# Kernel optimization log

Hardware: AMD Instinct MI355X
Metric: run time of the kernel (lower is better)

Reference implementation:

```python
import math
import jax, jax.numpy as jnp
import numpy as np

BLOCK = 256
LAYER_IDX = 5
NUM_HIDDEN_LAYERS = 32


def get_slopes(head_dim):
    equ = lambda x: 1 / 2 ** (8 / x)
    log2 = math.log2(head_dim)
    if log2.is_integer():
        return [equ(head_dim) ** i for i in range(1, head_dim + 1)]
    lower = 2 ** math.floor(log2)
    upper = 2 ** math.ceil(log2)
    ls = get_slopes(lower)
    us = get_slopes(upper)
    return ls + us[::2][: head_dim - lower]


def setup_inputs() -> dict:
    key = jax.random.key(0)
    k1, k2, k3 = jax.random.split(key, 3)
    B, H, S, D = 2, 64, 4096, 64
    q = jax.random.normal(k1, (B, H, S, D), dtype=jnp.float32)
    k = jax.random.normal(k2, (B, H, S, D), dtype=jnp.float32)
    v = jax.random.normal(k3, (B, H, S, D), dtype=jnp.float32)
    mask = jnp.ones((B, S), dtype=jnp.int32)
    return {"query_states": q, "key_states": k, "value_states": v, "attention_mask": mask}


def _lightning_attention(q, k, v, attention_mask):
    B, H, S, D = q.shape
    E = v.shape[-1]
    # mask padded positions in values
    v = v * attention_mask[:, None, :, None].astype(v.dtype)

    # per-head decay slopes, scaled by layer depth (note: H == D by construction)
    slopes = np.asarray(get_slopes(D), dtype=np.float32)
    slopes = slopes * (1.0 - LAYER_IDX / (NUM_HIDDEN_LAYERS - 1) + 1e-05)
    slope = jnp.asarray(slopes)[:, None, None]  # [H, 1, 1]

    arr = jnp.arange(1, BLOCK + 1, dtype=jnp.float32)
    q_decay = jnp.exp(-slope * arr[:, None])            # [H, BLOCK, 1]
    k_decay = jnp.exp(-slope * (BLOCK - arr)[:, None])  # [H, BLOCK, 1]
    idx = arr[:, None] - arr[None, :]                   # [BLOCK, BLOCK]
    s_idx = slope * idx[None]                           # [H, BLOCK, BLOCK] (slope [H,1,1] broadcasts)
    diag_decay = jnp.exp(jnp.where(idx[None] >= 0, -s_idx, -jnp.inf))  # [H, BLOCK, BLOCK]
    block_decay = jnp.exp(-slope * BLOCK)               # [H, 1, 1]

    nb = S // BLOCK
    qb = q.reshape(B, H, nb, BLOCK, D).transpose(2, 0, 1, 3, 4)  # [nb, B, H, BLOCK, D]
    kb = k.reshape(B, H, nb, BLOCK, D).transpose(2, 0, 1, 3, 4)
    vb = v.reshape(B, H, nb, BLOCK, E).transpose(2, 0, 1, 3, 4)

    def step(kv, blk):
        qi, ki, vi = blk  # each [B, H, BLOCK, D/E]
        # inter-block: decayed query reads recurrent kv state
        o_inter = jnp.einsum('bhmd,bhde->bhme', qi * q_decay, kv)
        # intra-block: causal decayed attention within the block
        qk = jnp.einsum('bhmd,bhnd->bhmn', qi, ki) * diag_decay
        o_intra = jnp.einsum('bhmn,bhne->bhme', qk, vi)
        # update recurrent state
        kv_new = block_decay * kv + jnp.einsum('bhmd,bhme->bhde', ki * k_decay, vi)
        return kv_new, o_inter + o_intra

    kv0 = jnp.zeros((B, H, D, E), dtype=jnp.float32)
    _, outs = jax.lax.scan(step, kv0, (qb, kb, vb))  # outs: [nb, B, H, BLOCK, E]
    out = outs.transpose(1, 2, 0, 3, 4).reshape(B, H, S, E)
    return out


def reference(query_states, key_states, value_states, attention_mask):
    return _lightning_attention(query_states, key_states, value_states, attention_mask)
```

## Files before the change

kernel.cpp:

```cpp
#include <hip/hip_runtime.h>

typedef __attribute__((ext_vector_type(4))) float f4;
typedef __attribute__((ext_vector_type(4))) float f32x4;
typedef __attribute__((ext_vector_type(8))) short short8;
typedef __attribute__((ext_vector_type(4))) short short4v;
typedef __attribute__((ext_vector_type(4))) unsigned int uint4v;

#define S_  4096
#define NB_ 16
#define SLOPE_SCALE 0.838719677419355f

__device__ __forceinline__ float slope_for_head(int h) {
    return exp2f(-(float)(h + 1) * 0.125f) * SLOPE_SCALE;
}

__device__ __forceinline__ short f2bf(float f) {
    unsigned u = __float_as_uint(f);
    u += 0x7FFFu + ((u >> 16) & 1u);
    return (short)(u >> 16);
}

__global__ __launch_bounds__(256, 4) void phase1_kvblocks(
    const float* __restrict__ k, const float* __restrict__ v,
    const int* __restrict__ mask, float* __restrict__ kvt,
    short* __restrict__ vt)
{
    __shared__ float ks[64][68];
    __shared__ float vs[64][68];
    const int j  = blockIdx.x;
    const int bh = blockIdx.y;
    const int b  = bh >> 6;
    const int h  = bh & 63;
    const int t  = threadIdx.x;
    const float slope = slope_for_head(h);
    const int e  = t >> 2;
    const int dg = (t & 3) << 4;

    const f32x4 zf = {0.f, 0.f, 0.f, 0.f};
    f4 acc[4];
    acc[0] = zf; acc[1] = zf; acc[2] = zf; acc[3] = zf;

    const long long tilebase = ((long long)bh * S_ + j * 256) * 64;

    for (int c = 0; c < 4; ++c) {
        for (int i = 0; i < 4; ++i) {
            int fi  = t + i * 256;
            int row = fi >> 4;
            int col = (fi & 15) << 2;
            long long g = tilebase + (long long)(c * 64 + row) * 64 + col;
            *(f4*)&ks[row][col] = *(const f4*)(k + g);
            f4 vv = *(const f4*)(v + g);
            float mv = (float)mask[b * S_ + j * 256 + c * 64 + row];
            vv *= mv;
            *(f4*)&vs[row][col] = vv;
        }
        __syncthreads();

        for (int n = 0; n < 64; ++n) {
            float kd = __expf(-slope * (float)(255 - (c * 64 + n)));
            float a  = vs[n][e] * kd;
            const f4* krow = (const f4*)&ks[n][dg];
            acc[0] += a * krow[0];
            acc[1] += a * krow[1];
            acc[2] += a * krow[2];
            acc[3] += a * krow[3];
        }

        {
            int nb = (t & 3) << 4;
            unsigned w[8];
            for (int i = 0; i < 8; ++i) {
                unsigned lo = (unsigned short)f2bf(vs[nb + 2 * i][e]);
                unsigned hi = (unsigned short)f2bf(vs[nb + 2 * i + 1][e]);
                w[i] = lo | (hi << 16);
            }
            long long g = ((long long)(bh * 64 + e)) * S_ + j * 256 + c * 64 + nb;
            uint4v* dst = (uint4v*)(vt + g);
            uint4v w0 = {w[0], w[1], w[2], w[3]};
            uint4v w1 = {w[4], w[5], w[6], w[7]};
            dst[0] = w0;
            dst[1] = w1;
        }
        __syncthreads();
    }

    float* o = kvt + ((long long)(bh * NB_ + j)) * 4096 + e * 64 + dg;
    *(f4*)(o + 0)  = acc[0];
    *(f4*)(o + 4)  = acc[1];
    *(f4*)(o + 8)  = acc[2];
    *(f4*)(o + 12) = acc[3];
}

__global__ __launch_bounds__(256) void phase2_scan(float* __restrict__ kvt)
{
    const int bh = blockIdx.x;
    const int h  = bh & 63;
    const int t  = threadIdx.x;
    const float slope = slope_for_head(h);
    const float bd = __expf(-slope * 256.0f);

    const f32x4 zf = {0.f, 0.f, 0.f, 0.f};
    f4 st[4];
    st[0] = zf; st[1] = zf; st[2] = zf; st[3] = zf;

    f4* base = (f4*)(kvt + (long long)bh * NB_ * 4096);
    for (int j = 0; j < NB_; ++j) {
        f4* p = base + j * 1024;
        for (int i = 0; i < 4; ++i) {
            f4 tmp = p[t + i * 256];
            p[t + i * 256] = st[i];
            st[i] = st[i] * bd + tmp;
        }
    }
}

__global__ __launch_bounds__(256, 2) void phase3_output(
    const float* __restrict__ q, const float* __restrict__ k,
    const float* __restrict__ kvt, const short* __restrict__ vt,
    float* __restrict__ out)
{
    __shared__ short P[4][64 * 56];
    const int j    = blockIdx.x;
    const int bh   = blockIdx.y;
    const int h    = bh & 63;
    const int tid  = threadIdx.x;
    const int wave = tid >> 6;
    const int lane = tid & 63;
    const int quad = lane >> 4;
    const int l16  = lane & 15;
    const int wrole  = (wave + j) & 3;
    const float slope = slope_for_head(h);
    const int mwbase = wrole << 6;

    const long long rowbase = (long long)bh * S_ + j * 256 + mwbase;

    short8 qf[4][2];
    for (int mt = 0; mt < 4; ++mt) {
        const float* qp = q + (rowbase + mt * 16 + l16) * 64 + quad * 8;
        for (int ks = 0; ks < 2; ++ks) {
            f4 a = *(const f4*)(qp + ks * 32);
            f4 b = *(const f4*)(qp + ks * 32 + 4);
            short8 f;
            f[0] = f2bf(a.x); f[1] = f2bf(a.y); f[2] = f2bf(a.z); f[3] = f2bf(a.w);
            f[4] = f2bf(b.x); f[5] = f2bf(b.y); f[6] = f2bf(b.z); f[7] = f2bf(b.w);
            qf[mt][ks] = f;
        }
    }

    const f32x4 zf = {0.f, 0.f, 0.f, 0.f};
    f32x4 of[4][4];
    for (int et = 0; et < 4; ++et)
        for (int mt = 0; mt < 4; ++mt) of[et][mt] = zf;

    const float* kvp = kvt + ((long long)(bh * NB_ + j) << 12);
    for (int et = 0; et < 4; ++et) {
        for (int ks = 0; ks < 2; ++ks) {
            const float* p = kvp + (et * 16 + l16) * 64 + ks * 32 + quad * 8;
            f4 a = *(const f4*)(p);
            f4 b = *(const f4*)(p + 4);
            short8 af;
            af[0] = f2bf(a.x); af[1] = f2bf(a.y); af[2] = f2bf(a.z); af[3] = f2bf(a.w);
            af[4] = f2bf(b.x); af[5] = f2bf(b.y); af[6] = f2bf(b.z); af[7] = f2bf(b.w);
            for (int mt = 0; mt < 4; ++mt)
                of[et][mt] = __builtin_amdgcn_mfma_f32_16x16x32_bf16(
                    af, qf[mt][ks], of[et][mt], 0, 0, 0);
        }
    }
    for (int mt = 0; mt < 4; ++mt) {
        float qd = __expf(-slope * (float)(mwbase + mt * 16 + l16 + 1));
        for (int et = 0; et < 4; ++et) of[et][mt] *= qd;
    }

    const float er1 = __expf(slope);
    const float er2 = er1 * er1;
    const float er3 = er2 * er1;
    short* Pw = &P[wave][0];
    const int nchunks = (mwbase >> 5) + 2;

    for (int c = 0; c < nchunks; ++c) {
        const int nbase = c << 5;

        short8 kf[2][2];
        for (int nt = 0; nt < 2; ++nt) {
            const float* kp = k + ((long long)bh * S_ + j * 256 + nbase + nt * 16 + l16) * 64 + quad * 8;
            for (int ks = 0; ks < 2; ++ks) {
                f4 a = *(const f4*)(kp + ks * 32);
                f4 b = *(const f4*)(kp + ks * 32 + 4);
                short8 f;
                f[0] = f2bf(a.x); f[1] = f2bf(a.y); f[2] = f2bf(a.z); f[3] = f2bf(a.w);
                f[4] = f2bf(b.x); f[5] = f2bf(b.y); f[6] = f2bf(b.z); f[7] = f2bf(b.w);
                kf[nt][ks] = f;
            }
        }

        f32x4 sf[2][4];
        for (int nt = 0; nt < 2; ++nt)
            for (int mt = 0; mt < 4; ++mt) sf[nt][mt] = zf;
        for (int nt = 0; nt < 2; ++nt)
            for (int ks = 0; ks < 2; ++ks)
                for (int mt = 0; mt < 4; ++mt)
                    sf[nt][mt] = __builtin_amdgcn_mfma_f32_16x16x32_bf16(
                        kf[nt][ks], qf[mt][ks], sf[nt][mt], 0, 0, 0);

        for (int nt = 0; nt < 2; ++nt) {
            for (int mt = 0; mt < 4; ++mt) {
                int n0 = nbase + nt * 16 + quad * 4;
                int m  = mwbase + mt * 16 + l16;
                float ddb = __expf(-slope * (float)(m - n0));
                f32x4 s = sf[nt][mt];
                float v0 = (m >= n0)     ? s[0] * ddb       : 0.f;
                float v1 = (m >= n0 + 1) ? s[1] * ddb * er1 : 0.f;
                float v2 = (m >= n0 + 2) ? s[2] * ddb * er2 : 0.f;
                float v3 = (m >= n0 + 3) ? s[3] * ddb * er3 : 0.f;
                short4v pk = {f2bf(v0), f2bf(v1), f2bf(v2), f2bf(v3)};
                *(short4v*)&Pw[(mt * 16 + l16) * 56 + nt * 16 + quad * 4] = pk;
            }
        }
        asm volatile("s_waitcnt lgkmcnt(0)" ::: "memory");

        short8 pb[4];
        for (int mt = 0; mt < 4; ++mt)
            pb[mt] = *(const short8*)&Pw[(mt * 16 + l16) * 56 + quad * 8];
        short8 va[4];
        for (int et = 0; et < 4; ++et)
            va[et] = *(const short8*)(vt + ((long long)(bh * 64 + et * 16 + l16)) * S_
                                         + j * 256 + nbase + quad * 8);

        for (int et = 0; et < 4; ++et)
            for (int mt = 0; mt < 4; ++mt)
                of[et][mt] = __builtin_amdgcn_mfma_f32_16x16x32_bf16(
                    va[et], pb[mt], of[et][mt], 0, 0, 0);
    }

    for (int mt = 0; mt < 4; ++mt) {
        float* orow = out + (rowbase + mt * 16 + l16) * 64;
        for (int et = 0; et < 4; ++et) {
            f4 o = {of[et][mt][0], of[et][mt][1], of[et][mt][2], of[et][mt][3]};
            *(f4*)(orow + et * 16 + quad * 4) = o;
        }
    }
}

extern "C" void kernel_launch(void* const* d_in, const int* in_sizes, int n_in,
                              void* d_out, int out_size, void* d_ws, size_t ws_size,
                              hipStream_t stream) {
    const float* q    = (const float*)d_in[0];
    const float* k    = (const float*)d_in[1];
    const float* v    = (const float*)d_in[2];
    const int*   mask = (const int*)d_in[3];
    float* kvt = (float*)d_ws;
    short* vt  = (short*)((char*)d_ws + (size_t)128 * 16 * 4096 * 4);
    float* out = (float*)d_out;

    phase1_kvblocks<<<dim3(16, 128), 256, 0, stream>>>(k, v, mask, kvt, vt);
    phase2_scan<<<128, 256, 0, stream>>>(kvt);
    phase3_output<<<dim3(16, 128), 256, 0, stream>>>(q, k, kvt, vt, out);
}
```

Before: 546.5 us.

## Use split-bf16 MFMA for KV blocks, cache bf16 K, split output waves

Phase 1 now computes the per-block K^T V state with MFMA, using a hi/lo bf16 split (three products) to keep near-fp32 accuracy. The k-decay is folded into the shared-memory load, and V^T is stored in a chunk-tiled layout. When the workspace is large enough, phase 1 also writes a bf16 copy of K so phase 3 skips reconverting it. Phase 2 spreads the scan over four times as many blocks and loads all 16 states up front. Phase 3 runs one wave per block with independent row roles, which trades shared-memory reuse for finer scheduling and costs extra writes of the bf16 K copy.

```diff
diff --git a/kernel.cpp b/kernel.cpp
--- a/kernel.cpp
+++ b/kernel.cpp
@@ -19,28 +19,32 @@
     u += 0x7FFFu + ((u >> 16) & 1u);
     return (short)(u >> 16);
 }
-
+__device__ __forceinline__ float bf2f(short s) {
+    return __uint_as_float(((unsigned)(unsigned short)s) << 16);
+}
+
+template<int USE_KBF>
 __global__ __launch_bounds__(256, 4) void phase1_kvblocks(
     const float* __restrict__ k, const float* __restrict__ v,
     const int* __restrict__ mask, float* __restrict__ kvt,
-    short* __restrict__ vt)
+    short* __restrict__ vt, short* __restrict__ kbf)
 {
-    __shared__ float ks[64][68];
-    __shared__ float vs[64][68];
+    __shared__ float ks[64][69];
+    __shared__ float vs[64][69];
     const int j  = blockIdx.x;
     const int bh = blockIdx.y;
     const int b  = bh >> 6;
     const int h  = bh & 63;
     const int t  = threadIdx.x;
+    const int wave = t >> 6, lane = t & 63, quad = lane >> 4, l16 = lane & 15;
     const float slope = slope_for_head(h);
-    const int e  = t >> 2;
-    const int dg = (t & 3) << 4;
 
     const f32x4 zf = {0.f, 0.f, 0.f, 0.f};
-    f4 acc[4];
+    f32x4 acc[4];
     acc[0] = zf; acc[1] = zf; acc[2] = zf; acc[3] = zf;
 
     const long long tilebase = ((long long)bh * S_ + j * 256) * 64;
+    const long long vtbase   = ((long long)(bh * NB_ + j)) * 16384;
 
     for (int c = 0; c < 4; ++c) {
         for (int i = 0; i < 4; ++i) {
@@ -48,95 +52,122 @@
             int row = fi >> 4;
             int col = (fi & 15) << 2;
             long long g = tilebase + (long long)(c * 64 + row) * 64 + col;
-            *(f4*)&ks[row][col] = *(const f4*)(k + g);
+            f4 kk = *(const f4*)(k + g);
+            if (USE_KBF) {
+                short4v kb = { f2bf(kk.x), f2bf(kk.y), f2bf(kk.z), f2bf(kk.w) };
+                *(short4v*)(kbf + g) = kb;
+            }
+            float kd = __expf(-slope * (float)(255 - (c * 64 + row)));
+            *(f4*)&ks[row][col] = kk * kd;
             f4 vv = *(const f4*)(v + g);
             float mv = (float)mask[b * S_ + j * 256 + c * 64 + row];
-            vv *= mv;
-            *(f4*)&vs[row][col] = vv;
+            *(f4*)&vs[row][col] = vv * mv;
         }
         __syncthreads();
 
-        for (int n = 0; n < 64; ++n) {
-            float kd = __expf(-slope * (float)(255 - (c * 64 + n)));
-            float a  = vs[n][e] * kd;
-            const f4* krow = (const f4*)&ks[n][dg];
-            acc[0] += a * krow[0];
-            acc[1] += a * krow[1];
-            acc[2] += a * krow[2];
-            acc[3] += a * krow[3];
-        }
-
         {
+            int e  = t >> 2;
             int nb = (t & 3) << 4;
             unsigned w[8];
-            for (int i = 0; i < 8; ++i) {
-                unsigned lo = (unsigned short)f2bf(vs[nb + 2 * i][e]);
-                unsigned hi = (unsigned short)f2bf(vs[nb + 2 * i + 1][e]);
-                w[i] = lo | (hi << 16);
-            }
-            long long g = ((long long)(bh * 64 + e)) * S_ + j * 256 + c * 64 + nb;
+            #pragma unroll
+            for (int i2 = 0; i2 < 8; ++i2) {
+                unsigned lo = (unsigned short)f2bf(vs[nb + 2 * i2][e]);
+                unsigned hi = (unsigned short)f2bf(vs[nb + 2 * i2 + 1][e]);
+                w[i2] = lo | (hi << 16);
+            }
+            long long g = vtbase + (long long)(c * 2 + (nb >> 5)) * 2048
+                        + e * 32 + (nb & 31);
             uint4v* dst = (uint4v*)(vt + g);
             uint4v w0 = {w[0], w[1], w[2], w[3]};
             uint4v w1 = {w[4], w[5], w[6], w[7]};
-            dst[0] = w0;
-            dst[1] = w1;
+            dst[0] = w0; dst[1] = w1;
+        }
+
+        #pragma unroll
+        for (int cc = 0; cc < 2; ++cc) {
+            const int nb32 = cc * 32;
+            short8 ahi, alo;
+            #pragma unroll
+            for (int jj = 0; jj < 8; ++jj) {
+                float x = vs[nb32 + quad * 8 + jj][wave * 16 + l16];
+                short hi = f2bf(x);
+                ahi[jj] = hi;
+                alo[jj] = f2bf(x - bf2f(hi));
+            }
+            #pragma unroll
+            for (int dt = 0; dt < 4; ++dt) {
+                short8 bhi, blo;
+                #pragma unroll
+                for (int jj = 0; jj < 8; ++jj) {
+                    float x = ks[nb32 + quad * 8 + jj][dt * 16 + l16];
+                    short hi = f2bf(x);
+                    bhi[jj] = hi;
+                    blo[jj] = f2bf(x - bf2f(hi));
+                }
+                acc[dt] = __builtin_amdgcn_mfma_f32_16x16x32_bf16(ahi, bhi, acc[dt], 0, 0, 0);
+                acc[dt] = __builtin_amdgcn_mfma_f32_16x16x32_bf16(ahi, blo, acc[dt], 0, 0, 0);
+                acc[dt] = __builtin_amdgcn_mfma_f32_16x16x32_bf16(alo, bhi, acc[dt], 0, 0, 0);
+            }
         }
         __syncthreads();
     }
 
-    float* o = kvt + ((long long)(bh * NB_ + j)) * 4096 + e * 64 + dg;
-    *(f4*)(o + 0)  = acc[0];
-    *(f4*)(o + 4)  = acc[1];
-    *(f4*)(o + 8)  = acc[2];
-    *(f4*)(o + 12) = acc[3];
+    float* o = kvt + ((long long)(bh * NB_ + j)) * 4096;
+    #pragma unroll
+    for (int dt = 0; dt < 4; ++dt) {
+        #pragma unroll
+        for (int r = 0; r < 4; ++r) {
+            int e = wave * 16 + quad * 4 + r;
+            o[e * 64 + dt * 16 + l16] = acc[dt][r];
+        }
+    }
 }
 
 __global__ __launch_bounds__(256) void phase2_scan(float* __restrict__ kvt)
 {
-    const int bh = blockIdx.x;
-    const int h  = bh & 63;
-    const int t  = threadIdx.x;
+    const int g    = blockIdx.x;
+    const int bh   = g >> 2;
+    const int part = g & 3;
+    const int h    = bh & 63;
     const float slope = slope_for_head(h);
     const float bd = __expf(-slope * 256.0f);
 
-    const f32x4 zf = {0.f, 0.f, 0.f, 0.f};
-    f4 st[4];
-    st[0] = zf; st[1] = zf; st[2] = zf; st[3] = zf;
-
-    f4* base = (f4*)(kvt + (long long)bh * NB_ * 4096);
-    for (int j = 0; j < NB_; ++j) {
-        f4* p = base + j * 1024;
-        for (int i = 0; i < 4; ++i) {
-            f4 tmp = p[t + i * 256];
-            p[t + i * 256] = st[i];
-            st[i] = st[i] * bd + tmp;
-        }
-    }
-}
-
-__global__ __launch_bounds__(256, 2) void phase3_output(
-    const float* __restrict__ q, const float* __restrict__ k,
-    const float* __restrict__ kvt, const short* __restrict__ vt,
-    float* __restrict__ out)
+    f4* base = (f4*)(kvt + (long long)bh * NB_ * 4096) + part * 256 + threadIdx.x;
+    f4 vals[NB_];
+    #pragma unroll
+    for (int jj = 0; jj < NB_; ++jj) vals[jj] = base[jj * 1024];
+    f4 st = {0.f, 0.f, 0.f, 0.f};
+    #pragma unroll
+    for (int jj = 0; jj < NB_; ++jj) {
+        base[jj * 1024] = st;
+        st = st * bd + vals[jj];
+    }
+}
+
+template<int USE_KBF>
+__global__ __launch_bounds__(64, 4) void phase3_output(
+    const float* __restrict__ q, const float* __restrict__ kfp,
+    const short* __restrict__ kbf, const float* __restrict__ kvt,
+    const short* __restrict__ vt, float* __restrict__ out)
 {
-    __shared__ short P[4][64 * 56];
-    const int j    = blockIdx.x;
+    __shared__ short P[64 * 56];
+    const int role = blockIdx.x & 3;
+    const int j    = blockIdx.x >> 2;
     const int bh   = blockIdx.y;
     const int h    = bh & 63;
-    const int tid  = threadIdx.x;
-    const int wave = tid >> 6;
-    const int lane = tid & 63;
+    const int lane = threadIdx.x;
     const int quad = lane >> 4;
     const int l16  = lane & 15;
-    const int wrole  = (wave + j) & 3;
     const float slope = slope_for_head(h);
-    const int mwbase = wrole << 6;
+    const int mwbase = role << 6;
 
     const long long rowbase = (long long)bh * S_ + j * 256 + mwbase;
 
     short8 qf[4][2];
+    #pragma unroll
     for (int mt = 0; mt < 4; ++mt) {
         const float* qp = q + (rowbase + mt * 16 + l16) * 64 + quad * 8;
+        #pragma unroll
         for (int ks = 0; ks < 2; ++ks) {
             f4 a = *(const f4*)(qp + ks * 32);
             f4 b = *(const f4*)(qp + ks * 32 + 4);
@@ -149,11 +180,15 @@
 
     const f32x4 zf = {0.f, 0.f, 0.f, 0.f};
     f32x4 of[4][4];
+    #pragma unroll
     for (int et = 0; et < 4; ++et)
+        #pragma unroll
         for (int mt = 0; mt < 4; ++mt) of[et][mt] = zf;
 
     const float* kvp = kvt + ((long long)(bh * NB_ + j) << 12);
+    #pragma unroll
     for (int et = 0; et < 4; ++et) {
+        #pragma unroll
         for (int ks = 0; ks < 2; ++ks) {
             const float* p = kvp + (et * 16 + l16) * 64 + ks * 32 + quad * 8;
             f4 a = *(const f4*)(p);
@@ -161,48 +196,78 @@
             short8 af;
             af[0] = f2bf(a.x); af[1] = f2bf(a.y); af[2] = f2bf(a.z); af[3] = f2bf(a.w);
             af[4] = f2bf(b.x); af[5] = f2bf(b.y); af[6] = f2bf(b.z); af[7] = f2bf(b.w);
+            #pragma unroll
             for (int mt = 0; mt < 4; ++mt)
                 of[et][mt] = __builtin_amdgcn_mfma_f32_16x16x32_bf16(
                     af, qf[mt][ks], of[et][mt], 0, 0, 0);
         }
     }
+    #pragma unroll
     for (int mt = 0; mt < 4; ++mt) {
         float qd = __expf(-slope * (float)(mwbase + mt * 16 + l16 + 1));
+        #pragma unroll
         for (int et = 0; et < 4; ++et) of[et][mt] *= qd;
     }
 
     const float er1 = __expf(slope);
     const float er2 = er1 * er1;
     const float er3 = er2 * er1;
-    short* Pw = &P[wave][0];
     const int nchunks = (mwbase >> 5) + 2;
+    const long long kTile = ((long long)bh * S_ + j * 256) * 64;
+    const long long vTile = ((long long)(bh * NB_ + j)) * 16384;
 
     for (int c = 0; c < nchunks; ++c) {
         const int nbase = c << 5;
 
+        short8 va[4];
+        #pragma unroll
+        for (int et = 0; et < 4; ++et)
+            va[et] = *(const short8*)(vt + vTile + c * 2048
+                                      + (et * 16 + l16) * 32 + quad * 8);
+
         short8 kf[2][2];
-        for (int nt = 0; nt < 2; ++nt) {
-            const float* kp = k + ((long long)bh * S_ + j * 256 + nbase + nt * 16 + l16) * 64 + quad * 8;
-            for (int ks = 0; ks < 2; ++ks) {
-                f4 a = *(const f4*)(kp + ks * 32);
-                f4 b = *(const f4*)(kp + ks * 32 + 4);
-                short8 f;
-                f[0] = f2bf(a.x); f[1] = f2bf(a.y); f[2] = f2bf(a.z); f[3] = f2bf(a.w);
-                f[4] = f2bf(b.x); f[5] = f2bf(b.y); f[6] = f2bf(b.z); f[7] = f2bf(b.w);
-                kf[nt][ks] = f;
+        if (USE_KBF) {
+            #pragma unroll
+            for (int nt = 0; nt < 2; ++nt) {
+                const short* kp = kbf + kTile
+                    + (long long)(nbase + nt * 16 + l16) * 64 + quad * 8;
+                kf[nt][0] = *(const short8*)(kp);
+                kf[nt][1] = *(const short8*)(kp + 32);
+            }
+        } else {
+            #pragma unroll
+            for (int nt = 0; nt < 2; ++nt) {
+                const float* kp = kfp + kTile
+                    + (long long)(nbase + nt * 16 + l16) * 64 + quad * 8;
+                #pragma unroll
+                for (int ks = 0; ks < 2; ++ks) {
+                    f4 a = *(const f4*)(kp + ks * 32);
+                    f4 b = *(const f4*)(kp + ks * 32 + 4);
+                    short8 f;
+                    f[0] = f2bf(a.x); f[1] = f2bf(a.y); f[2] = f2bf(a.z); f[3] = f2bf(a.w);
+                    f[4] = f2bf(b.x); f[5] = f2bf(b.y); f[6] = f2bf(b.z); f[7] = f2bf(b.w);
+                    kf[nt][ks] = f;
+                }
             }
         }
 
         f32x4 sf[2][4];
+        #pragma unroll
         for (int nt = 0; nt < 2; ++nt)
+            #pragma unroll
             for (int mt = 0; mt < 4; ++mt) sf[nt][mt] = zf;
+        #pragma unroll
         for (int nt = 0; nt < 2; ++nt)
+            #pragma unroll
             for (int ks = 0; ks < 2; ++ks)
+                #pragma unroll
                 for (int mt = 0; mt < 4; ++mt)
                     sf[nt][mt] = __builtin_amdgcn_mfma_f32_16x16x32_bf16(
                         kf[nt][ks], qf[mt][ks], sf[nt][mt], 0, 0, 0);
 
+        #pragma unroll
         for (int nt = 0; nt < 2; ++nt) {
+            #pragma unroll
             for (int mt = 0; mt < 4; ++mt) {
                 int n0 = nbase + nt * 16 + quad * 4;
                 int m  = mwbase + mt * 16 + l16;
@@ -213,27 +278,28 @@
                 float v2 = (m >= n0 + 2) ? s[2] * ddb * er2 : 0.f;
                 float v3 = (m >= n0 + 3) ? s[3] * ddb * er3 : 0.f;
                 short4v pk = {f2bf(v0), f2bf(v1), f2bf(v2), f2bf(v3)};
-                *(short4v*)&Pw[(mt * 16 + l16) * 56 + nt * 16 + quad * 4] = pk;
+                *(short4v*)&P[(mt * 16 + l16) * 56 + nt * 16 + quad * 4] = pk;
             }
         }
         asm volatile("s_waitcnt lgkmcnt(0)" ::: "memory");
 
         short8 pb[4];
+        #pragma unroll
         for (int mt = 0; mt < 4; ++mt)
-            pb[mt] = *(const short8*)&Pw[(mt * 16 + l16) * 56 + quad * 8];
-        short8 va[4];
+            pb[mt] = *(const short8*)&P[(mt * 16 + l16) * 56 + quad * 8];
+
+        #pragma unroll
         for (int et = 0; et < 4; ++et)
-            va[et] = *(const short8*)(vt + ((long long)(bh * 64 + et * 16 + l16)) * S_
-                                         + j * 256 + nbase + quad * 8);
-
-        for (int et = 0; et < 4; ++et)
+            #pragma unroll
             for (int mt = 0; mt < 4; ++mt)
                 of[et][mt] = __builtin_amdgcn_mfma_f32_16x16x32_bf16(
                     va[et], pb[mt], of[et][mt], 0, 0, 0);
     }
 
+    #pragma unroll
     for (int mt = 0; mt < 4; ++mt) {
         float* orow = out + (rowbase + mt * 16 + l16) * 64;
+        #pragma unroll
         for (int et = 0; et < 4; ++et) {
             f4 o = {of[et][mt][0], of[et][mt][1], of[et][mt][2], of[et][mt][3]};
             *(f4*)(orow + et * 16 + quad * 4) = o;
@@ -249,10 +315,18 @@
     const float* v    = (const float*)d_in[2];
     const int*   mask = (const int*)d_in[3];
     float* kvt = (float*)d_ws;
-    short* vt  = (short*)((char*)d_ws + (size_t)128 * 16 * 4096 * 4);
+    short* vt  = (short*)((char*)d_ws + (size_t)33554432);
+    short* kbf = (short*)((char*)d_ws + (size_t)33554432 + 67108864);
     float* out = (float*)d_out;
 
-    phase1_kvblocks<<<dim3(16, 128), 256, 0, stream>>>(k, v, mask, kvt, vt);
-    phase2_scan<<<128, 256, 0, stream>>>(kvt);
-    phase3_output<<<dim3(16, 128), 256, 0, stream>>>(q, k, kvt, vt, out);
-}
+    const bool use_kbf = ws_size >= (size_t)167772160;
+    if (use_kbf) {
+        phase1_kvblocks<1><<<dim3(16, 128), 256, 0, stream>>>(k, v, mask, kvt, vt, kbf);
+        phase2_scan<<<512, 256, 0, stream>>>(kvt);
+        phase3_output<1><<<dim3(64, 128), 64, 0, stream>>>(q, k, kbf, kvt, vt, out);
+    } else {
+        phase1_kvblocks<0><<<dim3(16, 128), 256, 0, stream>>>(k, v, mask, kvt, vt, kbf);
+        phase2_scan<<<512, 256, 0, stream>>>(kvt);
+        phase3_output<0><<<dim3(64, 128), 64, 0, stream>>>(q, k, kbf, kvt, vt, out);
+    }
+}
```

New measurement: 696.6 us. 27.5% more time.
